# Performance work log

Hardware: AMD Instinct MI355X
Metric: run time of the kernel (lower is better)

Reference implementation:

```python
import jax, jax.numpy as jnp
import numpy as np

B, S, E, H = 2, 2048, 1280, 20
D = E // H  # head_dim = 64
SCALING = D ** -0.5


def setup_inputs() -> dict:
    key = jax.random.key(0)
    k1, k2, k3, k4, k5 = jax.random.split(key, 5)
    return {
        "hidden_states": jax.random.normal(k1, (B, S, E), dtype=jnp.float32),
        "qkv_w": jax.random.normal(k2, (E, 3 * E), dtype=jnp.float32) * (E ** -0.5),
        "qkv_b": jax.random.normal(k3, (3 * E,), dtype=jnp.float32) * 0.02,
        "out_w": jax.random.normal(k4, (E, E), dtype=jnp.float32) * (E ** -0.5),
        "out_b": jax.random.normal(k5, (E,), dtype=jnp.float32) * 0.02,
    }


def reference(hidden_states, qkv_w, qkv_b, out_w, out_b):
    b, s, e = hidden_states.shape
    # fused QKV projection
    qkv = hidden_states @ qkv_w + qkv_b              # [B,S,3E]
    q, k, v = jnp.split(qkv, 3, axis=-1)
    q = q * SCALING                                  # module pre-scales q; attn uses scaling=1.0
    q = q.reshape(b, s, H, D)
    k = k.reshape(b, s, H, D)
    v = v.reshape(b, s, H, D)
    scores = jnp.einsum("bqhd,bkhd->bhqk", q, k)     # [B,H,S,S]
    # decoder (causal) attention, per AttentionType.DECODER
    causal = jnp.tril(jnp.ones((s, s), dtype=bool))
    scores = jnp.where(causal[None, None], scores, jnp.finfo(scores.dtype).min)
    probs = jax.nn.softmax(scores, axis=-1)
    attn = jnp.einsum("bhqk,bkhd->bqhd", probs, v).reshape(b, s, e)
    return attn @ out_w + out_b
```

## Files before the change

### kernel.cpp

```cpp
#include <hip/hip_runtime.h>
#include <hip/hip_bf16.h>
#include <stdint.h>

typedef unsigned short u16;
typedef short s8v __attribute__((ext_vector_type(8)));
typedef float f32x4 __attribute__((ext_vector_type(4)));

#define NB 2
#define NH 20
#define SEQ 2048
#define EMB 1280
#define HD 64
#define MT (NB*SEQ)
#define N3E (3*EMB)
#define QSCALE 0.18033688011112042f

__device__ __forceinline__ u16 f2bf(float f){
  unsigned u = __float_as_uint(f);
  u += 0x7fffu + ((u >> 16) & 1u);
  return (u16)(u >> 16);
}

__device__ __forceinline__ unsigned pk2(float a, float b){
  __hip_bfloat162 h = __float22bfloat162_rn(float2{a, b});
  return *reinterpret_cast<unsigned*>(&h);
}

__global__ __launch_bounds__(256) void prep_kernel(
    const float* __restrict__ hs, const float* __restrict__ qkv_w,
    const float* __restrict__ out_w,
    u16* __restrict__ xb, u16* __restrict__ wqkvT, u16* __restrict__ woT)
{
  __shared__ float tl[32][33];
  int blk = blockIdx.x;
  if (blk < 5120){
    int i = blk*256 + threadIdx.x;
    float4 f = ((const float4* __restrict__)hs)[i];
    ushort4 o;
    o.x = f2bf(f.x); o.y = f2bf(f.y); o.z = f2bf(f.z); o.w = f2bf(f.w);
    ((ushort4*)xb)[i] = o;
    return;
  }
  const float* in; u16* out; int R, C, bx, by;
  if (blk < 9920){
    int b2 = blk - 5120; bx = b2 % 120; by = b2 / 120;
    in = qkv_w; out = wqkvT; R = EMB; C = N3E;
  } else {
    int b2 = blk - 9920; bx = b2 % 40; by = b2 / 40;
    in = out_w; out = woT; R = EMB; C = EMB;
  }
  int c0 = bx*32, r0 = by*32;
  int tx = threadIdx.x & 31, ty = threadIdx.x >> 5;
  #pragma unroll
  for (int i=0;i<4;i++)
    tl[ty + i*8][tx] = in[(size_t)(r0 + ty + i*8)*C + c0 + tx];
  __syncthreads();
  #pragma unroll
  for (int i=0;i<4;i++)
    out[(size_t)(c0 + ty + i*8)*R + r0 + tx] = f2bf(tl[tx][ty + i*8]);
}

template<int NIT>
__device__ __forceinline__ void stage_swz(const u16* gsrc, int ld, u16* lds, int t){
  #pragma unroll
  for (int i=0;i<NIT;i++){
    int f = i*256 + t;
    int row = f >> 3, sl = f & 7;
    int ssl = sl ^ (row & 7);
    __builtin_amdgcn_global_load_lds(
      (const __attribute__((address_space(1))) void*)(gsrc + (size_t)row*ld + ssl*8),
      (__attribute__((address_space(3))) void*)(lds + f*8), 16, 0, 0);
  }
}

__device__ __forceinline__ s8v frag_ld(const u16* lds, int row, int ks){
  int sl = ks ^ (row & 7);
  return *(const s8v*)(lds + row*64 + sl*8);
}

template<int EPI>
__global__ __launch_bounds__(256) void gemm_bt_kernel(
    const u16* __restrict__ A, const u16* __restrict__ Bt, const float* __restrict__ bias,
    float* __restrict__ Cout, int Ntot, int K,
    u16* __restrict__ qb, u16* __restrict__ kbf, u16* __restrict__ vT)
{
  __shared__ u16 As[2][128*64];
  __shared__ u16 Bs[2][128*64];
  int t = threadIdx.x;
  int lane = t & 63, w = t >> 6;
  int wr = w >> 1, wc = w & 1;
  int g = lane >> 4, c = lane & 15;
  int m0 = blockIdx.y*128, n0 = blockIdx.x*128;
  const u16* Ab = A  + (size_t)m0*K;
  const u16* Bb = Bt + (size_t)n0*K;
  f32x4 acc[4][4] = {};
  int NT = K/64;
  stage_swz<4>(Ab, K, As[0], t);
  stage_swz<4>(Bb, K, Bs[0], t);
  for (int kt = 0; kt < NT; ++kt){
    int d = kt & 1;
    if (kt < NT-1){
      int k1 = (kt+1)*64;
      stage_swz<4>(Ab + k1, K, As[d^1], t);
      stage_swz<4>(Bb + k1, K, Bs[d^1], t);
      asm volatile("s_waitcnt vmcnt(8)" ::: "memory");
    } else {
      asm volatile("s_waitcnt vmcnt(0)" ::: "memory");
    }
    __builtin_amdgcn_s_barrier();
    __builtin_amdgcn_sched_barrier(0);
    #pragma unroll
    for (int kb2=0;kb2<2;kb2++){
      s8v af[4], bfr[4];
      #pragma unroll
      for (int m=0;m<4;m++) af[m]  = frag_ld(As[d], wr*64 + m*16 + c, kb2*4 + g);
      #pragma unroll
      for (int n=0;n<4;n++) bfr[n] = frag_ld(Bs[d], wc*64 + n*16 + c, kb2*4 + g);
      #pragma unroll
      for (int m=0;m<4;m++)
        #pragma unroll
        for (int n=0;n<4;n++)
          acc[m][n] = __builtin_amdgcn_mfma_f32_16x16x32_bf16(af[m], bfr[n], acc[m][n], 0, 0, 0);
    }
    asm volatile("s_waitcnt lgkmcnt(0)" ::: "memory");
    __builtin_amdgcn_s_barrier();
  }
  #pragma unroll
  for (int m=0;m<4;m++){
    int growb = m0 + wr*64 + m*16 + g*4;
    #pragma unroll
    for (int n=0;n<4;n++){
      int gcol = n0 + wc*64 + n*16 + c;
      float bv = bias[gcol];
      if (EPI == 1){
        #pragma unroll
        for (int r=0;r<4;r++)
          Cout[(size_t)(growb + r)*Ntot + gcol] = acc[m][n][r] + bv;
      } else {
        int which = gcol / EMB;
        int e = gcol - which*EMB;
        int hh = e >> 6, d2 = e & 63;
        int bi = growb >> 11, sb = growb & 2047;
        size_t bh = (size_t)bi*NH + hh;
        if (which == 2){
          uint2 pv2;
          pv2.x = pk2(acc[m][n][0] + bv, acc[m][n][1] + bv);
          pv2.y = pk2(acc[m][n][2] + bv, acc[m][n][3] + bv);
          *(uint2*)(vT + (bh*HD + d2)*SEQ + sb) = pv2;
        } else {
          u16* dst = (which == 0) ? qb : kbf;
          float scl = (which == 0) ? QSCALE : 1.0f;
          #pragma unroll
          for (int r=0;r<4;r++)
            dst[(bh*SEQ + sb + r)*HD + d2] = f2bf((acc[m][n][r] + bv)*scl);
        }
      }
    }
  }
}

__global__ __launch_bounds__(256) void attn_kernel(
    const u16* __restrict__ qb, const u16* __restrict__ kbf, const u16* __restrict__ vT,
    u16* __restrict__ attn)
{
  __shared__ u16 Kls[2][64*64];
  __shared__ u16 Vls[2][64*64];
  __shared__ u16 Ps[4][1024];
  int bh = blockIdx.x;
  int b = bh / NH, h = bh - b*NH;
  int qt = 31 - blockIdx.y;
  int t = threadIdx.x, lane = t & 63, w = t >> 6;
  int g = lane >> 4, c = lane & 15;
  u16* pw = &Ps[w][0];
  const u16* Kb = kbf + (size_t)bh*SEQ*HD;
  const u16* Vb = vT  + (size_t)bh*HD*SEQ;

  int qwb = qt*64 + w*16;
  const u16* qrow = qb + ((size_t)bh*SEQ + qwb + c)*HD;
  s8v aq0 = *(const s8v*)(qrow + g*8);
  s8v aq1 = *(const s8v*)(qrow + 32 + g*8);
  f32x4 po[4] = {};
  float mrow = -1e30f, lrow = 0.f;
  int cswz = 2*(c & 7);

  stage_swz<2>(Kb, HD, Kls[0], t);
  stage_swz<2>(Vb, SEQ, Vls[0], t);

  for (int kt = 0; kt <= qt; ++kt){
    int cur = kt & 1;
    const u16* Ks = Kls[cur];
    const u16* Vs = Vls[cur];
    if (kt < qt){
      int k1 = (kt + 1)*64;
      stage_swz<2>(Kb + (size_t)k1*HD, HD,  Kls[cur^1], t);
      stage_swz<2>(Vb + k1,            SEQ, Vls[cur^1], t);
      asm volatile("s_waitcnt vmcnt(4)" ::: "memory");
    } else {
      asm volatile("s_waitcnt vmcnt(0)" ::: "memory");
    }
    __builtin_amdgcn_s_barrier();
    __builtin_amdgcn_sched_barrier(0);

    int k0 = kt*64;
    s8v vv[8];
    #pragma unroll
    for (int kb2=0;kb2<2;kb2++)
      #pragma unroll
      for (int dt=0;dt<4;dt++)
        vv[kb2*4+dt] = frag_ld(Vs, dt*16 + c, kb2*4 + g);
    f32x4 sc[4];
    __builtin_amdgcn_s_setprio(1);
    #pragma unroll
    for (int nt=0;nt<4;nt++){
      s8v k0f = frag_ld(Ks, nt*16 + c, g);
      s8v k1f = frag_ld(Ks, nt*16 + c, 4 + g);
      f32x4 z = {0.f,0.f,0.f,0.f};
      sc[nt] = __builtin_amdgcn_mfma_f32_16x16x32_bf16(k0f, aq0, z,      0,0,0);
      sc[nt] = __builtin_amdgcn_mfma_f32_16x16x32_bf16(k1f, aq1, sc[nt], 0,0,0);
    }
    __builtin_amdgcn_s_setprio(0);
    if (kt == qt){
      #pragma unroll
      for (int nt=0;nt<4;nt++){
        int kg = k0 + nt*16 + g*4;
        #pragma unroll
        for (int r=0;r<4;r++)
          if (kg + r > qwb + c) sc[nt][r] = -1e30f;
      }
    }
    float mt = fmaxf(fmaxf(sc[0][0],sc[0][1]), fmaxf(sc[0][2],sc[0][3]));
    #pragma unroll
    for (int nt=1;nt<4;nt++)
      mt = fmaxf(mt, fmaxf(fmaxf(sc[nt][0],sc[nt][1]), fmaxf(sc[nt][2],sc[nt][3])));
    mt = fmaxf(mt, __shfl_xor(mt, 16));
    mt = fmaxf(mt, __shfl_xor(mt, 32));
    if (!__all(mt - mrow <= 8.0f)){
      float mn = fmaxf(mrow, mt);
      float alpha = exp2f(mrow - mn);
      mrow = mn;
      lrow *= alpha;
      #pragma unroll
      for (int dt=0;dt<4;dt++)
        #pragma unroll
        for (int r=0;r<4;r++)
          po[dt][r] *= alpha;
    }
    float rs = 0.f;
    #pragma unroll
    for (int nt=0;nt<4;nt++)
      #pragma unroll
      for (int r=0;r<4;r++){
        float pe = exp2f(sc[nt][r] - mrow);
        sc[nt][r] = pe;
        rs += pe;
      }
    rs += __shfl_xor(rs, 16);
    rs += __shfl_xor(rs, 32);
    lrow += rs;
    #pragma unroll
    for (int nt=0;nt<4;nt++){
      uint2 pk;
      pk.x = pk2(sc[nt][0], sc[nt][1]);
      pk.y = pk2(sc[nt][2], sc[nt][3]);
      *(uint2*)(pw + c*64 + ((nt*4 + g) ^ cswz)*4) = pk;
    }
    __builtin_amdgcn_s_setprio(1);
    #pragma unroll
    for (int kb2=0;kb2<2;kb2++){
      s8v pa = *(const s8v*)(pw + c*64 + ((kb2*8 + 2*g) ^ cswz)*4);
      #pragma unroll
      for (int dt=0;dt<4;dt++)
        po[dt] = __builtin_amdgcn_mfma_f32_16x16x32_bf16(vv[kb2*4+dt], pa, po[dt], 0,0,0);
    }
    __builtin_amdgcn_s_setprio(0);
    asm volatile("s_waitcnt lgkmcnt(0)" ::: "memory");
    __builtin_amdgcn_s_barrier();
  }
  float inv = 1.0f / lrow;
  const size_t orow = ((size_t)(b*SEQ + qwb + c))*EMB + h*HD;
  #pragma unroll
  for (int dt=0;dt<4;dt++){
    uint2 o;
    o.x = pk2(po[dt][0]*inv, po[dt][1]*inv);
    o.y = pk2(po[dt][2]*inv, po[dt][3]*inv);
    *(uint2*)(attn + orow + dt*16 + g*4) = o;
  }
}

extern "C" void kernel_launch(void* const* d_in, const int* in_sizes, int n_in,
                              void* d_out, int out_size, void* d_ws, size_t ws_size,
                              hipStream_t stream) {
  const float* hs    = (const float*)d_in[0];
  const float* qkv_w = (const float*)d_in[1];
  const float* qkv_b = (const float*)d_in[2];
  const float* out_w = (const float*)d_in[3];
  const float* out_b = (const float*)d_in[4];
  float* out = (float*)d_out;

  char* p = (char*)d_ws;
  u16* xb    = (u16*)p; p += (size_t)MT*EMB*2;
  u16* wqkvT = (u16*)p; p += (size_t)N3E*EMB*2;
  u16* woT   = (u16*)p; p += (size_t)EMB*EMB*2;
  u16* qbuf  = (u16*)p; p += (size_t)NB*NH*SEQ*HD*2;
  u16* kbuf  = (u16*)p; p += (size_t)NB*NH*SEQ*HD*2;
  u16* vTb   = (u16*)p; p += (size_t)NB*NH*SEQ*HD*2;
  u16* attnb = (u16*)p; p += (size_t)MT*EMB*2;

  prep_kernel<<<11520, 256, 0, stream>>>(hs, qkv_w, out_w, xb, wqkvT, woT);
  gemm_bt_kernel<0><<<dim3(N3E/128, MT/128), 256, 0, stream>>>(
      xb, wqkvT, qkv_b, nullptr, N3E, EMB, qbuf, kbuf, vTb);
  attn_kernel<<<dim3(40, 32), 256, 0, stream>>>(qbuf, kbuf, vTb, attnb);
  gemm_bt_kernel<1><<<dim3(EMB/128, MT/128), 256, 0, stream>>>(
      attnb, woT, out_b, out, EMB, EMB, nullptr, nullptr, nullptr);
}
```

Before: 242.3 us.

## Replace QKV GEMM with 256x256 tiled 8-wave kernel with half-tile pipelining

The QKV projection moves from a 128x128 tile, 4-wave GEMM to a new 256x256 tile, 512-thread kernel. It stages A and B in halves, interleaved with four MFMA quadrant phases, and remaps blocks through a swizzled 1D grid of 240 blocks. The aim is higher arithmetic intensity per LDS byte and better overlap of global-to-LDS loads with MFMA work. The cost is a large LDS footprint (128 KB), higher register pressure and fewer blocks, which could hurt occupancy and load balance across CUs.

Result: faster. 229.9 us (-5.1%).

```diff
diff --git a/kernel.cpp b/kernel.cpp
--- a/kernel.cpp
+++ b/kernel.cpp
@@ -73,9 +73,176 @@
   }
 }
 
+__device__ __forceinline__ void stage_half(const u16* gsrc, int ld, u16* lds, int t){
+  #pragma unroll
+  for (int i=0;i<2;i++){
+    int f = i*512 + t;
+    int row = f >> 3, sl = f & 7;
+    int ssl = sl ^ (row & 7);
+    __builtin_amdgcn_global_load_lds(
+      (const __attribute__((address_space(1))) void*)(gsrc + (size_t)row*ld + ssl*8),
+      (__attribute__((address_space(3))) void*)(lds + f*8), 16, 0, 0);
+  }
+}
+
 __device__ __forceinline__ s8v frag_ld(const u16* lds, int row, int ks){
   int sl = ks ^ (row & 7);
   return *(const s8v*)(lds + row*64 + sl*8);
+}
+
+#define MFMA16(a,b,c) __builtin_amdgcn_mfma_f32_16x16x32_bf16(a,b,c,0,0,0)
+
+__global__ __launch_bounds__(512, 2) void gemm256_qkv_kernel(
+    const u16* __restrict__ A, const u16* __restrict__ Bt, const float* __restrict__ bias,
+    u16* __restrict__ qb, u16* __restrict__ kbf, u16* __restrict__ vT)
+{
+  const int K = EMB, NT = EMB/64;
+  __shared__ u16 As[2][256*64];
+  __shared__ u16 Bs[2][256*64];
+  int t = threadIdx.x;
+  int lane = t & 63, w = t >> 6;
+  int wr = w >> 2, wc = w & 3;
+  int g = lane >> 4, c = lane & 15;
+  int o = blockIdx.x;
+  int sw = (o & 7)*30 + (o >> 3);
+  int bxs = sw >> 4;
+  int bys = sw & 15;
+  int m0 = bys*256, n0 = bxs*256;
+  const u16* Ab = A  + (size_t)m0*K;
+  const u16* Bb = Bt + (size_t)n0*K;
+  f32x4 acc[8][4] = {};
+  s8v af[8], bf0[4], bf1[4];
+
+  stage_half(Ab,                        K, &As[0][0],        t);
+  stage_half(Bb,                        K, &Bs[0][0],        t);
+  stage_half(Ab + (size_t)128*K,        K, &As[0][128*64],   t);
+  stage_half(Bb + (size_t)128*K,        K, &Bs[0][128*64],   t);
+  stage_half(Ab + 64,                   K, &As[1][0],        t);
+  stage_half(Bb + 64,                   K, &Bs[1][0],        t);
+  asm volatile("s_waitcnt vmcnt(4)" ::: "memory");
+  __builtin_amdgcn_s_barrier();
+
+  for (int kt = 0; kt < NT; ++kt){
+    const int bcur = kt & 1, bnxt = bcur ^ 1;
+    const u16* Acur = &As[bcur][0];
+    const u16* Bcur = &Bs[bcur][0];
+    u16* AnH1 = &As[bnxt][128*64];
+    u16* BnH1 = &Bs[bnxt][128*64];
+    u16* AcH0 = &As[bcur][0];
+    u16* BcH0 = &Bs[bcur][0];
+    const int ko1 = (kt+1)*64, ko2 = (kt+2)*64;
+    const bool s1 = (kt+1 < NT), s2 = (kt+2 < NT);
+
+    #pragma unroll
+    for (int m=0;m<4;m++)
+      #pragma unroll
+      for (int ks=0;ks<2;ks++)
+        af[m*2+ks] = frag_ld(Acur, wr*64 + m*16 + c, ks*4 + g);
+    #pragma unroll
+    for (int n=0;n<2;n++)
+      #pragma unroll
+      for (int ks=0;ks<2;ks++)
+        bf0[n*2+ks] = frag_ld(Bcur, wc*32 + n*16 + c, ks*4 + g);
+    if (s1) stage_half(Ab + (size_t)128*K + ko1, K, AnH1, t);
+    __builtin_amdgcn_s_barrier();
+    asm volatile("s_waitcnt lgkmcnt(0)" ::: "memory");
+    __builtin_amdgcn_sched_barrier(0);
+    __builtin_amdgcn_s_setprio(1);
+    #pragma unroll
+    for (int m=0;m<4;m++)
+      #pragma unroll
+      for (int n=0;n<2;n++)
+        #pragma unroll
+        for (int ks=0;ks<2;ks++)
+          acc[m][n] = MFMA16(af[m*2+ks], bf0[n*2+ks], acc[m][n]);
+    __builtin_amdgcn_s_setprio(0);
+    __builtin_amdgcn_s_barrier();
+
+    #pragma unroll
+    for (int n=0;n<2;n++)
+      #pragma unroll
+      for (int ks=0;ks<2;ks++)
+        bf1[n*2+ks] = frag_ld(Bcur, 128 + wc*32 + n*16 + c, ks*4 + g);
+    if (s1) stage_half(Bb + (size_t)128*K + ko1, K, BnH1, t);
+    __builtin_amdgcn_s_barrier();
+    asm volatile("s_waitcnt lgkmcnt(0)" ::: "memory");
+    __builtin_amdgcn_sched_barrier(0);
+    __builtin_amdgcn_s_setprio(1);
+    #pragma unroll
+    for (int m=0;m<4;m++)
+      #pragma unroll
+      for (int n=0;n<2;n++)
+        #pragma unroll
+        for (int ks=0;ks<2;ks++)
+          acc[m][n+2] = MFMA16(af[m*2+ks], bf1[n*2+ks], acc[m][n+2]);
+    __builtin_amdgcn_s_setprio(0);
+    __builtin_amdgcn_s_barrier();
+
+    #pragma unroll
+    for (int m=0;m<4;m++)
+      #pragma unroll
+      for (int ks=0;ks<2;ks++)
+        af[m*2+ks] = frag_ld(Acur, 128 + wr*64 + m*16 + c, ks*4 + g);
+    if (s2) stage_half(Ab + ko2, K, AcH0, t);
+    __builtin_amdgcn_s_barrier();
+    asm volatile("s_waitcnt lgkmcnt(0)" ::: "memory");
+    __builtin_amdgcn_sched_barrier(0);
+    __builtin_amdgcn_s_setprio(1);
+    #pragma unroll
+    for (int m=0;m<4;m++)
+      #pragma unroll
+      for (int n=0;n<2;n++)
+        #pragma unroll
+        for (int ks=0;ks<2;ks++)
+          acc[m+4][n] = MFMA16(af[m*2+ks], bf0[n*2+ks], acc[m+4][n]);
+    __builtin_amdgcn_s_setprio(0);
+    __builtin_amdgcn_s_barrier();
+
+    if (s2) stage_half(Bb + ko2, K, BcH0, t);
+    if (kt >= NT-3) asm volatile("s_waitcnt vmcnt(0)" ::: "memory");
+    else            asm volatile("s_waitcnt vmcnt(4)" ::: "memory");
+    __builtin_amdgcn_s_barrier();
+    __builtin_amdgcn_sched_barrier(0);
+    __builtin_amdgcn_s_setprio(1);
+    #pragma unroll
+    for (int m=0;m<4;m++)
+      #pragma unroll
+      for (int n=0;n<2;n++)
+        #pragma unroll
+        for (int ks=0;ks<2;ks++)
+          acc[m+4][n+2] = MFMA16(af[m*2+ks], bf1[n*2+ks], acc[m+4][n+2]);
+    __builtin_amdgcn_s_setprio(0);
+    __builtin_amdgcn_s_barrier();
+  }
+
+  #pragma unroll
+  for (int m=0;m<8;m++){
+    int arow = (m<4) ? (wr*64 + m*16) : (128 + wr*64 + (m-4)*16);
+    int growb = m0 + arow + g*4;
+    #pragma unroll
+    for (int n=0;n<4;n++){
+      int bcol = (n<2) ? (wc*32 + n*16) : (128 + wc*32 + (n-2)*16);
+      int gcol = n0 + bcol + c;
+      float bv = bias[gcol];
+      int which = gcol / EMB;
+      int e = gcol - which*EMB;
+      int hh = e >> 6, d2 = e & 63;
+      int bi = growb >> 11, sb = growb & 2047;
+      size_t bh = (size_t)bi*NH + hh;
+      if (which == 2){
+        uint2 pv2;
+        pv2.x = pk2(acc[m][n][0] + bv, acc[m][n][1] + bv);
+        pv2.y = pk2(acc[m][n][2] + bv, acc[m][n][3] + bv);
+        *(uint2*)(vT + (bh*HD + d2)*SEQ + sb) = pv2;
+      } else {
+        u16* dst = (which == 0) ? qb : kbf;
+        float scl = (which == 0) ? QSCALE : 1.0f;
+        #pragma unroll
+        for (int r=0;r<4;r++)
+          dst[(bh*SEQ + sb + r)*HD + d2] = f2bf((acc[m][n][r] + bv)*scl);
+      }
+    }
+  }
 }
 
 template<int EPI>
@@ -120,7 +287,7 @@
       for (int m=0;m<4;m++)
         #pragma unroll
         for (int n=0;n<4;n++)
-          acc[m][n] = __builtin_amdgcn_mfma_f32_16x16x32_bf16(af[m], bfr[n], acc[m][n], 0, 0, 0);
+          acc[m][n] = MFMA16(af[m], bfr[n], acc[m][n]);
     }
     asm volatile("s_waitcnt lgkmcnt(0)" ::: "memory");
     __builtin_amdgcn_s_barrier();
@@ -215,8 +382,8 @@
       s8v k0f = frag_ld(Ks, nt*16 + c, g);
       s8v k1f = frag_ld(Ks, nt*16 + c, 4 + g);
       f32x4 z = {0.f,0.f,0.f,0.f};
-      sc[nt] = __builtin_amdgcn_mfma_f32_16x16x32_bf16(k0f, aq0, z,      0,0,0);
-      sc[nt] = __builtin_amdgcn_mfma_f32_16x16x32_bf16(k1f, aq1, sc[nt], 0,0,0);
+      sc[nt] = MFMA16(k0f, aq0, z);
+      sc[nt] = MFMA16(k1f, aq1, sc[nt]);
     }
     __builtin_amdgcn_s_setprio(0);
     if (kt == qt){
@@ -270,7 +437,7 @@
       s8v pa = *(const s8v*)(pw + c*64 + ((kb2*8 + 2*g) ^ cswz)*4);
       #pragma unroll
       for (int dt=0;dt<4;dt++)
-        po[dt] = __builtin_amdgcn_mfma_f32_16x16x32_bf16(vv[kb2*4+dt], pa, po[dt], 0,0,0);
+        po[dt] = MFMA16(vv[kb2*4+dt], pa, po[dt]);
     }
     __builtin_amdgcn_s_setprio(0);
     asm volatile("s_waitcnt lgkmcnt(0)" ::: "memory");
@@ -307,8 +474,8 @@
   u16* attnb = (u16*)p; p += (size_t)MT*EMB*2;
 
   prep_kernel<<<11520, 256, 0, stream>>>(hs, qkv_w, out_w, xb, wqkvT, woT);
-  gemm_bt_kernel<0><<<dim3(N3E/128, MT/128), 256, 0, stream>>>(
-      xb, wqkvT, qkv_b, nullptr, N3E, EMB, qbuf, kbuf, vTb);
+  gemm256_qkv_kernel<<<240, 512, 0, stream>>>(
+      xb, wqkvT, qkv_b, qbuf, kbuf, vTb);
   attn_kernel<<<dim3(40, 32), 256, 0, stream>>>(qbuf, kbuf, vTb, attnb);
   gemm_bt_kernel<1><<<dim3(EMB/128, MT/128), 256, 0, stream>>>(
       attnb, woT, out_b, out, EMB, EMB, nullptr, nullptr, nullptr);
```
